# Optimization experiments

Measured on AMD Instinct MI355X. Metric: run time of the kernel, lower is better.

Reference implementation:

```python
import jax, jax.numpy as jnp
import numpy as np

M = 0.25      # margin m
GAMMA = 64.0  # scale gamma
N, D = 8192, 128
NUM_CLASSES = 512


def setup_inputs() -> dict:
    key = jax.random.key(0)
    k1, k2 = jax.random.split(key)
    inputs = jax.random.normal(k1, (N, D), dtype=jnp.float32)
    targets = jax.random.randint(k2, (N,), 0, NUM_CLASSES, dtype=jnp.int64)
    return {"inputs": inputs, "targets": targets}


def reference(inputs, targets):
    # L2-normalize rows -> cosine similarity matrix [n, n]
    x = inputs / jnp.linalg.norm(inputs, axis=1, keepdims=True)
    sim = x @ x.T
    # positive mask: same label (includes diagonal, matching the torch code)
    mask = targets[:, None] == targets[None, :]

    Op, On = 1.0 + M, -M
    delta_p, delta_n = 1.0 - M, M

    sim_d = jax.lax.stop_gradient(sim)  # .detach() in torch
    ap = jnp.maximum(Op - sim_d, 0.0)
    an = jnp.maximum(sim_d + On, 0.0)

    logit_p = -ap * (sim - delta_p) * GAMMA
    logit_n = an * (sim - delta_n) * GAMMA

    neg_inf = jnp.float32(-jnp.inf)
    # per-row logsumexp over positives of -logit_p, over negatives of logit_n
    lp = jax.nn.logsumexp(jnp.where(mask, -logit_p, neg_inf), axis=1)
    ln = jax.nn.logsumexp(jnp.where(mask, neg_inf, logit_n), axis=1)

    return jnp.mean(jax.nn.softplus(ln + lp))
```

## Files before the change

kernel.cpp:

```cpp
#include <hip/hip_runtime.h>
#include <math.h>


#define NR    8192
#define DIMK  128
#define NT    64
#define NBLKS 512
#define NCLS  512
#define MAXC  96

#define CE1 9.6089795f
#define CE0 -2.4022449f

typedef __attribute__((ext_vector_type(8))) short short8;
typedef __attribute__((ext_vector_type(4))) float f32x4;
typedef __attribute__((address_space(3))) uint32_t lds_u32;
typedef const __attribute__((address_space(1))) uint32_t glb_u32;

__device__ __forceinline__ unsigned short bf16_rne(float f) {
  uint32_t u = __float_as_uint(f);
  u += 0x7FFFu + ((u >> 16) & 1u);
  return (unsigned short)(u >> 16);
}

__device__ __forceinline__ float fexp2(float x) {
#if __has_builtin(__builtin_amdgcn_exp2f)
  return __builtin_amdgcn_exp2f(x);
#else
  return exp2f(x);
#endif
}


__global__ __launch_bounds__(256) void normalize_split_kernel(
    const float* __restrict__ x, unsigned short* __restrict__ xhi,
    unsigned short* __restrict__ xlo, float* __restrict__ gN,
    int* __restrict__ counter) {
  if (blockIdx.x < 32) gN[blockIdx.x * 256 + threadIdx.x] = 0.f;
  if (blockIdx.x == 32 && threadIdx.x == 0) *counter = 0;

  const int wave = threadIdx.x >> 6;
  const int lane = threadIdx.x & 63;
  const int l32  = lane & 31;
  const int row  = blockIdx.x * 8 + wave * 2 + (lane >> 5);
  const float4 v = ((const float4*)(x + (size_t)row * DIMK))[l32];
  float ss = v.x * v.x + v.y * v.y + v.z * v.z + v.w * v.w;
  #pragma unroll
  for (int s = 1; s < 32; s <<= 1) ss += __shfl_xor(ss, s);
  const float r = rsqrtf(ss);
  const float a0 = v.x * r, a1 = v.y * r, a2 = v.z * r, a3 = v.w * r;
  ushort4 hi, lo;
  hi.x = bf16_rne(a0); hi.y = bf16_rne(a1);
  hi.z = bf16_rne(a2); hi.w = bf16_rne(a3);
  lo.x = bf16_rne(a0 - __uint_as_float((uint32_t)hi.x << 16));
  lo.y = bf16_rne(a1 - __uint_as_float((uint32_t)hi.y << 16));
  lo.z = bf16_rne(a2 - __uint_as_float((uint32_t)hi.z << 16));
  lo.w = bf16_rne(a3 - __uint_as_float((uint32_t)hi.w << 16));
  ((ushort4*)xhi)[(size_t)row * 32 + l32] = hi;
  ((ushort4*)xlo)[(size_t)row * 32 + l32] = lo;
}

__global__ __launch_bounds__(512, 2) void simloss_kernel(
    const unsigned short* __restrict__ xhi, const unsigned short* __restrict__ xlo,
    float* __restrict__ gN) {
  __shared__ unsigned short S[32768];
  __shared__ float colbuf[2][4][128];

  const int tid  = threadIdx.x;
  const int wave = tid >> 6, lane = tid & 63;
  const int wy = wave & 3, wx = wave >> 2;
  const int q = lane >> 4, mcol = lane & 15;
  const bool isStage = (wy == 1) || (wy == 2);
  const bool isFlush = (wy == 0);
  const int srank = (wy - 1) + wx * 2;

  const int p  = blockIdx.x >> 4;
  const int b  = blockIdx.x & 15;
  const int n1 = NT - p;
  const int t0 = (b * (NT + 1)) >> 4;
  const int t1 = ((b + 1) * (NT + 1)) >> 4;
  const int ntile = t1 - t0;
  const int p2 = NT - 1 - p;

  int cur_bi = (t0 < n1) ? p : p2;

  auto stageA = [&](int bi) {
    const unsigned short* gh = xhi + (size_t)bi * 128 * DIMK;
    const unsigned short* gl = xlo + (size_t)bi * 128 * DIMK;
    #pragma unroll
    for (int g = 0; g < 4; ++g) {
      const int r  = wave * 16 + g * 4 + (lane >> 4);
      const int sc = (lane & 15) ^ (r & 15);
      __builtin_amdgcn_global_load_lds((glb_u32*)(gh + (size_t)r * DIMK + sc * 8),
          (lds_u32*)&S[(wave * 16 + g * 4) * 128], 16, 0, 0);
      __builtin_amdgcn_global_load_lds((glb_u32*)(gl + (size_t)r * DIMK + sc * 8),
          (lds_u32*)&S[16384 + (wave * 16 + g * 4) * 128], 16, 0, 0);
    }
  };
  auto stageB = [&](int bj, int buf) {
    const unsigned short* gb = xhi + (size_t)bj * 128 * DIMK;
    unsigned short* dst = &S[buf * 16384];
    #pragma unroll
    for (int g = 0; g < 8; ++g) {
      const int r  = srank * 32 + g * 4 + (lane >> 4);
      const int sc = (lane & 15) ^ (r & 15);
      __builtin_amdgcn_global_load_lds((glb_u32*)(gb + (size_t)r * DIMK + sc * 8),
          (lds_u32*)&dst[(srank * 32 + g * 4) * 128], 16, 0, 0);
    }
  };

  short8 Ah[2][4], Al[2][4];
  auto extractA = [&]() {
    #pragma unroll
    for (int fr = 0; fr < 2; ++fr) {
      const int r = wy * 32 + fr * 16 + mcol;
      #pragma unroll
      for (int ks = 0; ks < 4; ++ks) {
        const int pc = (ks * 4 + q) ^ mcol;
        Ah[fr][ks] = *(const short8*)&S[r * 128 + pc * 8];
        Al[fr][ks] = *(const short8*)&S[16384 + r * 128 + pc * 8];
      }
    }
  };

  float rowN[2][4] = {{0.f}};
  auto flushRows = [&](int bi_) {
    #pragma unroll
    for (int fr = 0; fr < 2; ++fr)
      #pragma unroll
      for (int rg = 0; rg < 4; ++rg) {
        float vn = rowN[fr][rg];
        #pragma unroll
        for (int m2 = 1; m2 < 16; m2 <<= 1) vn += __shfl_xor(vn, m2);
        if (mcol == 0)
          atomicAdd(&gN[bi_ * 128 + wy * 32 + fr * 16 + q * 4 + rg], vn);
      }
  };

  stageA(cur_bi);
  __syncthreads();
  extractA();
  __builtin_amdgcn_s_waitcnt(49279);
  __builtin_amdgcn_s_barrier();
  if (isStage) stageB((t0 < n1) ? p + t0 : p2 + (t0 - n1), 0);

  int pbi = -1, pbj = -1;

  for (int tl = 0; tl < ntile; ++tl) {
    const int ix = t0 + tl;
    const int bi = (ix < n1) ? p : p2;
    const int bj = (ix < n1) ? p + ix : p2 + (ix - n1);

    if (bi != cur_bi) {
      flushRows(cur_bi);
      cur_bi = bi;
      stageA(cur_bi);
      __syncthreads();
      extractA();
      #pragma unroll
      for (int fr = 0; fr < 2; ++fr)
        #pragma unroll
        for (int rg = 0; rg < 4; ++rg) rowN[fr][rg] = 0.f;
      __builtin_amdgcn_s_waitcnt(49279);
      __builtin_amdgcn_s_barrier();
      if (isStage) stageB(bj, tl & 1);
    }

    if (isStage) __builtin_amdgcn_s_waitcnt(112);
    else         __builtin_amdgcn_s_waitcnt(49279);
    __builtin_amdgcn_s_barrier();

    if (isFlush && pbj >= 0 && pbj != pbi) {
      const int col = wx * 64 + lane;
      float sn = 0.f;
      #pragma unroll
      for (int w = 0; w < 4; ++w) sn += colbuf[(tl & 1) ^ 1][w][col];
      atomicAdd(&gN[pbj * 128 + col], sn);
    }

    if (tl + 1 < ntile) {
      const int ix2 = ix + 1;
      if ((ix2 < n1) == (ix < n1)) {
        const int bj2 = (ix2 < n1) ? p + ix2 : p2 + (ix2 - n1);
        if (isStage) stageB(bj2, (tl + 1) & 1);
      }
    }

    const unsigned short* Bb = &S[(tl & 1) * 16384];
    f32x4 acc[2][4];
    #pragma unroll
    for (int fr = 0; fr < 2; ++fr)
      #pragma unroll
      for (int fc = 0; fc < 4; ++fc)
        acc[fr][fc] = (f32x4){0.f, 0.f, 0.f, 0.f};
    #pragma unroll
    for (int ks = 0; ks < 4; ++ks) {
      short8 bh[4];
      #pragma unroll
      for (int fc = 0; fc < 4; ++fc) {
        const int rb = wx * 64 + fc * 16 + mcol;
        const int pc = (ks * 4 + q) ^ mcol;
        bh[fc] = *(const short8*)&Bb[rb * 128 + pc * 8];
      }
      #pragma unroll
      for (int fc = 0; fc < 4; ++fc) {
        acc[0][fc] = __builtin_amdgcn_mfma_f32_16x16x32_bf16(Ah[0][ks], bh[fc], acc[0][fc], 0, 0, 0);
        acc[1][fc] = __builtin_amdgcn_mfma_f32_16x16x32_bf16(Ah[1][ks], bh[fc], acc[1][fc], 0, 0, 0);
        acc[0][fc] = __builtin_amdgcn_mfma_f32_16x16x32_bf16(Al[0][ks], bh[fc], acc[0][fc], 0, 0, 0);
        acc[1][fc] = __builtin_amdgcn_mfma_f32_16x16x32_bf16(Al[1][ks], bh[fc], acc[1][fc], 0, 0, 0);
      }
    }

    float cN[4] = {0.f, 0.f, 0.f, 0.f};
#define EPILOGUE(DIAG_)                                                      \
    {                                                                        \
      _Pragma("unroll")                                                      \
      for (int fr = 0; fr < 2; ++fr) {                                       \
        _Pragma("unroll")                                                    \
        for (int rg = 0; rg < 4; ++rg) {                                     \
          float vn = 0.f;                                                    \
          _Pragma("unroll")                                                  \
          for (int fc = 0; fc < 4; ++fc) {                                   \
            const float s = acc[fr][fc][rg];                                 \
            const float u = fmaxf(fmaf(s, CE1, CE0), 0.f);                   \
            float e = fexp2(u * u);                                          \
            if (DIAG_) {                                                     \
              const int rl = wy * 32 + fr * 16 + q * 4 + rg;                 \
              const int cl = wx * 64 + fc * 16 + mcol;                       \
              e = (rl == cl) ? 0.f : e;                                      \
            }                                                                \
            vn += e;                                                         \
            cN[fc] += e;                                                     \
          }                                                                  \
          rowN[fr][rg] += vn;                                                \
        }                                                                    \
      }                                                                      \
    }
    if (bj == bi) EPILOGUE(true) else EPILOGUE(false)
#undef EPILOGUE

    #pragma unroll
    for (int fc = 0; fc < 4; ++fc) {
      cN[fc] += __shfl_xor(cN[fc], 16);
      cN[fc] += __shfl_xor(cN[fc], 32);
    }
    if (q == 0) {
      #pragma unroll
      for (int fc = 0; fc < 4; ++fc)
        colbuf[tl & 1][wy][wx * 64 + fc * 16 + mcol] = cN[fc];
    }

    pbi = bi; pbj = bj;
  }

  __builtin_amdgcn_s_waitcnt(49279);
  __builtin_amdgcn_s_barrier();
  if (isFlush && pbj >= 0 && pbj != pbi) {
    const int col = wx * 64 + lane;
    float sn = 0.f;
    #pragma unroll
    for (int w = 0; w < 4; ++w) sn += colbuf[(ntile - 1) & 1][w][col];
    atomicAdd(&gN[pbj * 128 + col], sn);
  }
  flushRows(cur_bi);
}

__global__ __launch_bounds__(256) void finalize_kernel(
    const unsigned short* __restrict__ xhi, const unsigned short* __restrict__ xlo,
    const int* __restrict__ tgt, const float* __restrict__ gN,
    float* __restrict__ gC, int* __restrict__ counter, float* __restrict__ out) {
  __shared__ float Sf[MAXC * 129];
  __shared__ float Pv[MAXC];
  __shared__ float Ncor[MAXC];
  __shared__ int midx[MAXC];
  __shared__ float red[256];
  __shared__ int scnt;
  __shared__ int islast;

  const int tid = threadIdx.x;
  const int me  = (int)blockIdx.x;

  if (tid == 0) scnt = 0;
  if (tid < MAXC) { Pv[tid] = 0.f; Ncor[tid] = 0.f; }
  __syncthreads();

  const int4* t4 = (const int4*)tgt;
  for (int v = tid; v < NR / 4; v += 256) {
    const int4 tv = t4[v];
    const int base = v * 4;
    if (tv.x == me) { const int s_ = atomicAdd(&scnt, 1); if (s_ < MAXC) midx[s_] = base; }
    if (tv.y == me) { const int s_ = atomicAdd(&scnt, 1); if (s_ < MAXC) midx[s_] = base + 1; }
    if (tv.z == me) { const int s_ = atomicAdd(&scnt, 1); if (s_ < MAXC) midx[s_] = base + 2; }
    if (tv.w == me) { const int s_ = atomicAdd(&scnt, 1); if (s_ < MAXC) midx[s_] = base + 3; }
  }
  __syncthreads();
  const int m = (scnt < MAXC) ? scnt : MAXC;

  for (int v = tid; v < m * 32; v += 256) {
    const int r = v >> 5, c4 = v & 31;
    const int row = midx[r];
    const ushort4 h = ((const ushort4*)(xhi + (size_t)row * DIMK))[c4];
    const ushort4 l = ((const ushort4*)(xlo + (size_t)row * DIMK))[c4];
    float* d = &Sf[r * 129 + c4 * 4];
    d[0] = __uint_as_float((uint32_t)h.x << 16) + __uint_as_float((uint32_t)l.x << 16);
    d[1] = __uint_as_float((uint32_t)h.y << 16) + __uint_as_float((uint32_t)l.y << 16);
    d[2] = __uint_as_float((uint32_t)h.z << 16) + __uint_as_float((uint32_t)l.z << 16);
    d[3] = __uint_as_float((uint32_t)h.w << 16) + __uint_as_float((uint32_t)l.w << 16);
  }
  __syncthreads();

  for (int pr = tid; pr < m * m; pr += 256) {
    const int i = pr / m, j = pr - i * m;
    const float* vi = &Sf[i * 129];
    const float* vj = &Sf[j * 129];
    float s = 0.f;
    #pragma unroll 8
    for (int d = 0; d < 128; ++d) s = fmaf(vi[d], vj[d], s);
    const float ep = __expf(fmaxf(1.25f - s, 0.f) * fmaf(s, 64.f, -48.f));
    atomicAdd(&Pv[i], ep);
    if (i != j) {
      const float u = fmaxf(fmaf(s, CE1, CE0), 0.f);
      atomicAdd(&Ncor[i], fexp2(u * u));
    }
  }
  __syncthreads();

  float local = 0.f;
  for (int r = tid; r < m; r += 256) {
    const int gi = midx[r];
    local += log1pf(Pv[r] * (gN[gi] - Ncor[r]));
  }
  red[tid] = local;
  __syncthreads();
  #pragma unroll
  for (int s2 = 128; s2 > 0; s2 >>= 1) {
    if (tid < s2) red[tid] += red[tid + s2];
    __syncthreads();
  }
  if (tid == 0) atomicExch(&gC[me], red[0]);

  __builtin_amdgcn_s_waitcnt(0);
  __syncthreads();
  if (tid == 0) islast = (atomicAdd(counter, 1) == NCLS - 1) ? 1 : 0;
  __syncthreads();
  if (islast) {
    float sum = 0.f;
    #pragma unroll
    for (int u = 0; u < 2; ++u)
      sum += atomicAdd(&gC[tid * 2 + u], 0.0f);
    red[tid] = sum;
    __syncthreads();
    #pragma unroll
    for (int s2 = 128; s2 > 0; s2 >>= 1) {
      if (tid < s2) red[tid] += red[tid + s2];
      __syncthreads();
    }
    if (tid == 0) out[0] = red[0] / (float)NR;
  }
}

extern "C" void kernel_launch(void* const* d_in, const int* in_sizes, int n_in,
                              void* d_out, int out_size, void* d_ws, size_t ws_size,
                              hipStream_t stream) {
  const float* x  = (const float*)d_in[0];
  const int* tgt  = (const int*)d_in[1];
  float* out      = (float*)d_out;

  unsigned short* xhi = (unsigned short*)d_ws;
  unsigned short* xlo = xhi + (size_t)NR * DIMK;
  float* gN = (float*)((char*)d_ws + (size_t)NR * DIMK * 4);
  float* gC = gN + NR;
  int* counter = (int*)(gC + NCLS);

  normalize_split_kernel<<<NR / 8, 256, 0, stream>>>(x, xhi, xlo, gN, counter);
  simloss_kernel<<<NBLKS, 512, 0, stream>>>(xhi, xlo, gN);
  finalize_kernel<<<NCLS, 256, 0, stream>>>(xhi, xlo, tgt, gN, gC, counter, out);
}
```

Baseline: 111.3 us.

## Replace global atomic accumulation of negative sums with partial buffers reduced in finalize

The similarity kernel now writes per-block row and column partial sums into dedicated slots of a workspace buffer instead of atomically adding them into a shared per-row accumulator. The finalize kernel gathers and sums these partials only for the rows of its class. This removes contended global atomics and the zeroing pass in the normalize kernel. In exchange it uses more workspace, adds scattered reads in finalize, and moves finalize to 512-thread blocks.

```diff
diff --git a/kernel.cpp b/kernel.cpp
--- a/kernel.cpp
+++ b/kernel.cpp
@@ -34,10 +34,8 @@
 
 __global__ __launch_bounds__(256) void normalize_split_kernel(
     const float* __restrict__ x, unsigned short* __restrict__ xhi,
-    unsigned short* __restrict__ xlo, float* __restrict__ gN,
-    int* __restrict__ counter) {
-  if (blockIdx.x < 32) gN[blockIdx.x * 256 + threadIdx.x] = 0.f;
-  if (blockIdx.x == 32 && threadIdx.x == 0) *counter = 0;
+    unsigned short* __restrict__ xlo, int* __restrict__ counter) {
+  if (blockIdx.x == 0 && threadIdx.x == 0) *counter = 0;
 
   const int wave = threadIdx.x >> 6;
   const int lane = threadIdx.x & 63;
@@ -62,7 +60,7 @@
 
 __global__ __launch_bounds__(512, 2) void simloss_kernel(
     const unsigned short* __restrict__ xhi, const unsigned short* __restrict__ xlo,
-    float* __restrict__ gN) {
+    float* __restrict__ Col, float* __restrict__ Row) {
   __shared__ unsigned short S[32768];
   __shared__ float colbuf[2][4][128];
 
@@ -133,8 +131,16 @@
         #pragma unroll
         for (int m2 = 1; m2 < 16; m2 <<= 1) vn += __shfl_xor(vn, m2);
         if (mcol == 0)
-          atomicAdd(&gN[bi_ * 128 + wy * 32 + fr * 16 + q * 4 + rg], vn);
-      }
+          Row[(size_t)(b * 2 + wx) * NR + bi_ * 128 + wy * 32 + fr * 16 + q * 4 + rg] = vn;
+      }
+  };
+  auto zeroRows = [&](int bi_) {
+    #pragma unroll
+    for (int fr = 0; fr < 2; ++fr)
+      #pragma unroll
+      for (int rg = 0; rg < 4; ++rg)
+        if (mcol == 0)
+          Row[(size_t)(b * 2 + wx) * NR + bi_ * 128 + wy * 32 + fr * 16 + q * 4 + rg] = 0.f;
   };
 
   stageA(cur_bi);
@@ -175,7 +181,7 @@
       float sn = 0.f;
       #pragma unroll
       for (int w = 0; w < 4; ++w) sn += colbuf[(tl & 1) ^ 1][w][col];
-      atomicAdd(&gN[pbj * 128 + col], sn);
+      Col[(size_t)pbi * NR + pbj * 128 + col] = sn;
     }
 
     if (tl + 1 < ntile) {
@@ -260,20 +266,24 @@
     float sn = 0.f;
     #pragma unroll
     for (int w = 0; w < 4; ++w) sn += colbuf[(ntile - 1) & 1][w][col];
-    atomicAdd(&gN[pbj * 128 + col], sn);
+    Col[(size_t)pbi * NR + pbj * 128 + col] = sn;
   }
   flushRows(cur_bi);
-}
-
-__global__ __launch_bounds__(256) void finalize_kernel(
+  if (!(t0 < n1)) zeroRows(p);
+  if (!(t1 > n1)) zeroRows(p2);
+}
+
+__global__ __launch_bounds__(512) void finalize_kernel(
     const unsigned short* __restrict__ xhi, const unsigned short* __restrict__ xlo,
-    const int* __restrict__ tgt, const float* __restrict__ gN,
-    float* __restrict__ gC, int* __restrict__ counter, float* __restrict__ out) {
+    const int* __restrict__ tgt, const float* __restrict__ Col,
+    const float* __restrict__ Row, float* __restrict__ gC,
+    int* __restrict__ counter, float* __restrict__ out) {
   __shared__ float Sf[MAXC * 129];
   __shared__ float Pv[MAXC];
   __shared__ float Ncor[MAXC];
+  __shared__ float Gn[MAXC];
   __shared__ int midx[MAXC];
-  __shared__ float red[256];
+  __shared__ float red[512];
   __shared__ int scnt;
   __shared__ int islast;
 
@@ -281,11 +291,11 @@
   const int me  = (int)blockIdx.x;
 
   if (tid == 0) scnt = 0;
-  if (tid < MAXC) { Pv[tid] = 0.f; Ncor[tid] = 0.f; }
+  if (tid < MAXC) { Pv[tid] = 0.f; Ncor[tid] = 0.f; Gn[tid] = 0.f; }
   __syncthreads();
 
   const int4* t4 = (const int4*)tgt;
-  for (int v = tid; v < NR / 4; v += 256) {
+  for (int v = tid; v < NR / 4; v += 512) {
     const int4 tv = t4[v];
     const int base = v * 4;
     if (tv.x == me) { const int s_ = atomicAdd(&scnt, 1); if (s_ < MAXC) midx[s_] = base; }
@@ -296,7 +306,7 @@
   __syncthreads();
   const int m = (scnt < MAXC) ? scnt : MAXC;
 
-  for (int v = tid; v < m * 32; v += 256) {
+  for (int v = tid; v < m * 32; v += 512) {
     const int r = v >> 5, c4 = v & 31;
     const int row = midx[r];
     const ushort4 h = ((const ushort4*)(xhi + (size_t)row * DIMK))[c4];
@@ -307,9 +317,18 @@
     d[2] = __uint_as_float((uint32_t)h.z << 16) + __uint_as_float((uint32_t)l.z << 16);
     d[3] = __uint_as_float((uint32_t)h.w << 16) + __uint_as_float((uint32_t)l.w << 16);
   }
-  __syncthreads();
-
-  for (int pr = tid; pr < m * m; pr += 256) {
+  for (int v = tid; v < m * 96; v += 512) {
+    const int mi = v / 96, sl = v - mi * 96;
+    const int r = midx[mi];
+    const int pr = r >> 7;
+    float val;
+    if (sl < 64) val = (sl < pr) ? Col[(size_t)sl * NR + r] : 0.f;
+    else         val = Row[(size_t)(sl - 64) * NR + r];
+    if (val != 0.f) atomicAdd(&Gn[mi], val);
+  }
+  __syncthreads();
+
+  for (int pr = tid; pr < m * m; pr += 512) {
     const int i = pr / m, j = pr - i * m;
     const float* vi = &Sf[i * 129];
     const float* vj = &Sf[j * 129];
@@ -326,14 +345,12 @@
   __syncthreads();
 
   float local = 0.f;
-  for (int r = tid; r < m; r += 256) {
-    const int gi = midx[r];
-    local += log1pf(Pv[r] * (gN[gi] - Ncor[r]));
+  for (int r = tid; r < m; r += 512) {
+    local += log1pf(Pv[r] * (Gn[r] - Ncor[r]));
   }
   red[tid] = local;
   __syncthreads();
-  #pragma unroll
-  for (int s2 = 128; s2 > 0; s2 >>= 1) {
+  for (int s2 = 256; s2 > 0; s2 >>= 1) {
     if (tid < s2) red[tid] += red[tid + s2];
     __syncthreads();
   }
@@ -344,14 +361,9 @@
   if (tid == 0) islast = (atomicAdd(counter, 1) == NCLS - 1) ? 1 : 0;
   __syncthreads();
   if (islast) {
-    float sum = 0.f;
-    #pragma unroll
-    for (int u = 0; u < 2; ++u)
-      sum += atomicAdd(&gC[tid * 2 + u], 0.0f);
-    red[tid] = sum;
+    red[tid] = atomicAdd(&gC[tid], 0.0f);
     __syncthreads();
-    #pragma unroll
-    for (int s2 = 128; s2 > 0; s2 >>= 1) {
+    for (int s2 = 256; s2 > 0; s2 >>= 1) {
       if (tid < s2) red[tid] += red[tid + s2];
       __syncthreads();
     }
@@ -368,11 +380,12 @@
 
   unsigned short* xhi = (unsigned short*)d_ws;
   unsigned short* xlo = xhi + (size_t)NR * DIMK;
-  float* gN = (float*)((char*)d_ws + (size_t)NR * DIMK * 4);
-  float* gC = gN + NR;
+  float* Col = (float*)((char*)d_ws + (size_t)NR * DIMK * 4);
+  float* Row = Col + (size_t)64 * NR;
+  float* gC  = Row + (size_t)32 * NR;
   int* counter = (int*)(gC + NCLS);
 
-  normalize_split_kernel<<<NR / 8, 256, 0, stream>>>(x, xhi, xlo, gN, counter);
-  simloss_kernel<<<NBLKS, 512, 0, stream>>>(xhi, xlo, gN);
-  finalize_kernel<<<NCLS, 256, 0, stream>>>(xhi, xlo, tgt, gN, gC, counter, out);
-}
+  normalize_split_kernel<<<NR / 8, 256, 0, stream>>>(x, xhi, xlo, counter);
+  simloss_kernel<<<NBLKS, 512, 0, stream>>>(xhi, xlo, Col, Row);
+  finalize_kernel<<<NCLS, 512, 0, stream>>>(xhi, xlo, tgt, Col, Row, gC, counter, out);
+}
```

Measured after the change: 110.2 us. No clear change (-1.0%).
